# Kernel optimization log

Hardware: AMD Instinct MI355X
Metric: run time of the kernel (lower is better)

The kernel has to match this reference:

```python
import jax, jax.numpy as jnp
import numpy as np

B, N, C = 2, 2048, 768
H, HD = 12, 64
HID = 3072
LN_EPS = 1e-5
POL_EPS = 1e-6


def _layer_norm(x, g, b):
    m = jnp.mean(x, axis=-1, keepdims=True)
    v = jnp.mean(jnp.square(x - m), axis=-1, keepdims=True)
    return (x - m) * jax.lax.rsqrt(v + LN_EPS) * g + b


def _softmax_with_policy(attn, policy):
    # attn: [B,H,N,N], policy: [B,N,1]
    n = attn.shape[-1]
    ap = policy.reshape(policy.shape[0], 1, 1, n)  # [B,1,1,N]
    eye = jnp.eye(n, dtype=ap.dtype)[None, None]   # [1,1,N,N]
    ap = ap + (1.0 - ap) * eye                     # always attend to self
    attn = attn - jnp.max(attn, axis=-1, keepdims=True)
    attn = jnp.exp(attn.astype(jnp.float32)) * ap.astype(jnp.float32)
    attn = (attn + POL_EPS / n) / (jnp.sum(attn, axis=-1, keepdims=True) + POL_EPS)
    return attn


def setup_inputs() -> dict:
    key = jax.random.key(0)
    ks = jax.random.split(key, 12)
    s = lambda fan_in: 1.0 / np.sqrt(fan_in)
    x = jax.random.normal(ks[0], (B, N, C), dtype=jnp.float32)
    policy = (jax.random.uniform(ks[1], (B, N, 1)) > 0.5).astype(jnp.float32)
    return {
        "x": x,
        "policy": policy,
        "ln1_g": jnp.ones((C,), jnp.float32),
        "ln1_b": jnp.zeros((C,), jnp.float32),
        "qkv_w": jax.random.uniform(ks[2], (3 * H * HD, C), jnp.float32, -s(C), s(C)),
        "proj_w": jax.random.uniform(ks[3], (C, H * HD), jnp.float32, -s(H * HD), s(H * HD)),
        "proj_b": jnp.zeros((C,), jnp.float32),
        "ln2_g": jnp.ones((C,), jnp.float32),
        "ln2_b": jnp.zeros((C,), jnp.float32),
        "fc1_w": jax.random.uniform(ks[4], (HID, C), jnp.float32, -s(C), s(C)),
        "fc1_b": jnp.zeros((HID,), jnp.float32),
        "fc2_w": jax.random.uniform(ks[5], (C, HID), jnp.float32, -s(HID), s(HID)),
        "fc2_b": jnp.zeros((C,), jnp.float32),
    }


def reference(x, policy, ln1_g, ln1_b, qkv_w, proj_w, proj_b, ln2_g, ln2_b, fc1_w, fc1_b, fc2_w, fc2_b):
    b, n, c = x.shape
    scale = HD ** -0.5
    # --- attention branch (pre-LN) ---
    h = _layer_norm(x, ln1_g, ln1_b)
    qkv = (h @ qkv_w.T).reshape(b, n, 3, H, HD).transpose(2, 0, 3, 1, 4)  # [3,B,H,N,hd]
    q, k, v = qkv[0], qkv[1], qkv[2]
    attn = jnp.einsum("bhqd,bhkd->bhqk", q * scale, k)
    attn = _softmax_with_policy(attn, policy).astype(x.dtype)
    o = jnp.einsum("bhqk,bhkd->bhqd", attn, v).transpose(0, 2, 1, 3).reshape(b, n, H * HD)
    x = x + (o @ proj_w.T + proj_b)  # skip_lam = 1.0, dropout/drop_path = identity
    # --- MLP branch (pre-LN) ---
    h = _layer_norm(x, ln2_g, ln2_b)
    h = jax.nn.gelu(h @ fc1_w.T + fc1_b, approximate=False)  # torch nn.GELU = exact erf
    x = x + (h @ fc2_w.T + fc2_b)
    return x
```

## Files before the change

kernel.cpp:

```cpp
#include <hip/hip_runtime.h>

typedef unsigned short u16;
typedef unsigned int u32;
typedef float f32x4 __attribute__((ext_vector_type(4)));
typedef __bf16 bf16x8 __attribute__((ext_vector_type(8)));
typedef __bf16 bf16x4v __attribute__((ext_vector_type(4)));
typedef u16 u16x4v __attribute__((ext_vector_type(4)));
typedef u32 u32x2 __attribute__((ext_vector_type(2)));
typedef u32 u32x4 __attribute__((ext_vector_type(4)));

#define NHEAD 12
#define NN 2048
#define CC 768

#define GLOBAL_AS __attribute__((address_space(1)))
#define LDS_AS __attribute__((address_space(3)))

__device__ __forceinline__ u16 tobf(float f) {
  __bf16 h = (__bf16)f;
  return __builtin_bit_cast(u16, h);
}
__device__ __forceinline__ float bf2f(u16 h) {
  u32 u = ((u32)h) << 16;
  return __builtin_bit_cast(float, u);
}

#define N4_QKV 442368
#define N4_PROJ 147456
#define N4_FC 589824
__global__ __launch_bounds__(256) void cvt4_kernel(
    const float* __restrict__ a, const float* __restrict__ b,
    const float* __restrict__ c, const float* __restrict__ d,
    u16* __restrict__ oa, u16* __restrict__ ob, u16* __restrict__ oc,
    u16* __restrict__ od) {
  int i = blockIdx.x * 256 + threadIdx.x;
  const float* src;
  u16* dst;
  if (i < N4_QKV) {
    src = a; dst = oa;
  } else if (i < N4_QKV + N4_PROJ) {
    i -= N4_QKV; src = b; dst = ob;
  } else if (i < N4_QKV + N4_PROJ + N4_FC) {
    i -= N4_QKV + N4_PROJ; src = c; dst = oc;
  } else {
    i -= N4_QKV + N4_PROJ + N4_FC; src = d; dst = od;
    if (i >= N4_FC) return;
  }
  float4 v = ((const float4*)src)[i];
  u16x4v o = {tobf(v.x), tobf(v.y), tobf(v.z), tobf(v.w)};
  ((u16x4v*)dst)[i] = o;
}

__global__ __launch_bounds__(256) void ln_kernel(const float* __restrict__ x,
                                                 const float* __restrict__ gw,
                                                 const float* __restrict__ bw,
                                                 u16* __restrict__ out) {
  int row = blockIdx.x * 4 + (threadIdx.x >> 6);
  int lane = threadIdx.x & 63;
  const float* xr = x + (size_t)row * CC + lane * 12;
  float v[12];
  *(float4*)&v[0] = *(const float4*)(xr + 0);
  *(float4*)&v[4] = *(const float4*)(xr + 4);
  *(float4*)&v[8] = *(const float4*)(xr + 8);
  float s = 0.f, sq = 0.f;
#pragma unroll
  for (int j = 0; j < 12; ++j) { s += v[j]; sq += v[j] * v[j]; }
#pragma unroll
  for (int o = 1; o < 64; o <<= 1) { s += __shfl_xor(s, o); sq += __shfl_xor(sq, o); }
  float mean = s * (1.f / CC);
  float var = sq * (1.f / CC) - mean * mean;
  float rs = rsqrtf(var + 1e-5f);
  u16 ob[12];
#pragma unroll
  for (int j = 0; j < 12; ++j) {
    int c = lane * 12 + j;
    ob[j] = tobf((v[j] - mean) * rs * gw[c] + bw[c]);
  }
  u32* orow = (u32*)(out + (size_t)row * CC + lane * 12);
#pragma unroll
  for (int j = 0; j < 6; ++j) orow[j] = (u32)ob[2 * j] | ((u32)ob[2 * j + 1] << 16);
}

template <int BM, int OB, int HASB, int ACT, int RES>
__global__ __launch_bounds__(256) void gemm_kernel(
    const u16* __restrict__ A, const u16* __restrict__ Bw,
    const float* __restrict__ bias, const float* __restrict__ res,
    void* __restrict__ Cout, int M, int N, int K) {
  constexpr int MW = BM / 2;
  constexpr int MF = MW / 16;
  __shared__ __align__(16) u16 Alds[BM * 64];
  __shared__ __align__(16) u16 Blds[128 * 64];
  const int tid = threadIdx.x;
  const int lane = tid & 63, wave = tid >> 6;
  const int l15 = lane & 15, g = lane >> 4;
  const int bm = blockIdx.x * BM, bn = blockIdx.y * 128;
  const int wm = (wave >> 1) * MW, wn = (wave & 1) * 64;
  f32x4 acc[MF][4] = {};

  for (int kt = 0; kt < K; kt += 64) {
#pragma unroll
    for (int i = 0; i < BM / 32; ++i) {
      int ob_ = i * 4096 + wave * 1024;
      int lb = ob_ + lane * 16;
      int row = lb >> 7;
      int cb = (lb & 127) ^ ((row & 7) << 4);
      const u16* sa = A + (size_t)(bm + row) * K + kt + (cb >> 1);
      __builtin_amdgcn_global_load_lds((const GLOBAL_AS void*)sa,
                                       (LDS_AS void*)(Alds + (ob_ >> 1)), 16, 0, 0);
    }
#pragma unroll
    for (int i = 0; i < 4; ++i) {
      int ob_ = i * 4096 + wave * 1024;
      int lb = ob_ + lane * 16;
      int row = lb >> 7;
      int cb = (lb & 127) ^ ((row & 7) << 4);
      const u16* sb = Bw + (size_t)(bn + row) * K + kt + (cb >> 1);
      __builtin_amdgcn_global_load_lds((const GLOBAL_AS void*)sb,
                                       (LDS_AS void*)(Blds + (ob_ >> 1)), 16, 0, 0);
    }
    __syncthreads();
#pragma unroll
    for (int ks = 0; ks < 2; ++ks) {
      bf16x8 af[MF], bfr[4];
#pragma unroll
      for (int mi = 0; mi < MF; ++mi) {
        int row = wm + mi * 16 + l15;
        int cb = (ks * 64 + g * 16) ^ ((row & 7) << 4);
        af[mi] = *(const bf16x8*)&Alds[row * 64 + (cb >> 1)];
      }
#pragma unroll
      for (int ni = 0; ni < 4; ++ni) {
        int row = wn + ni * 16 + l15;
        int cb = (ks * 64 + g * 16) ^ ((row & 7) << 4);
        bfr[ni] = *(const bf16x8*)&Blds[row * 64 + (cb >> 1)];
      }
#pragma unroll
      for (int mi = 0; mi < MF; ++mi)
#pragma unroll
        for (int ni = 0; ni < 4; ++ni)
          acc[mi][ni] = __builtin_amdgcn_mfma_f32_16x16x32_bf16(af[mi], bfr[ni],
                                                                acc[mi][ni], 0, 0, 0);
    }
    __syncthreads();
  }
#pragma unroll
  for (int mi = 0; mi < MF; ++mi) {
#pragma unroll
    for (int ni = 0; ni < 4; ++ni) {
      int col = bn + wn + ni * 16 + l15;
      float bs = HASB ? bias[col] : 0.f;
#pragma unroll
      for (int r = 0; r < 4; ++r) {
        int rowm = bm + wm + mi * 16 + g * 4 + r;
        float v = acc[mi][ni][r] + bs;
        if (ACT) v = 0.5f * v * (1.f + erff(v * 0.70710678118654752f));
        if (RES) v += res[(size_t)rowm * N + col];
        if (OB)
          ((u16*)Cout)[(size_t)rowm * N + col] = tobf(v);
        else
          ((float*)Cout)[(size_t)rowm * N + col] = v;
      }
    }
  }
}

__global__ __launch_bounds__(256) void vsum_kernel(const u16* __restrict__ qkv,
                                                   float* __restrict__ vs) {
  int bh = blockIdx.x, q4 = blockIdx.y;
  int b = bh / NHEAD, h = bh % NHEAD;
  int d = threadIdx.x & 63, part = threadIdx.x >> 6;
  float s = 0.f;
  for (int n = q4 * 512 + part; n < q4 * 512 + 512; n += 4)
    s += bf2f(qkv[(size_t)(b * NN + n) * 2304 + 2 * CC + h * 64 + d]);
  __shared__ float red[256];
  red[threadIdx.x] = s;
  __syncthreads();
  if (threadIdx.x < 64) {
    float t = red[threadIdx.x] + red[threadIdx.x + 64] + red[threadIdx.x + 128] +
              red[threadIdx.x + 192];
    vs[q4 * (24 * 64) + bh * 64 + threadIdx.x] = t;
  }
}

#define SCL2E 0.18033688f
__global__ __launch_bounds__(256) void attn_kernel(const u16* __restrict__ qkv,
                                                   const float* __restrict__ policy,
                                                   const float* __restrict__ vsum,
                                                   u16* __restrict__ o) {
  __shared__ __align__(16) u16 Klds[2][64 * 64];
  __shared__ __align__(16) u16 Vlds[2][64 * 64];
  __shared__ __align__(16) u16 Plds[4][16 * 64];
  __shared__ float pol_lds[NN];
  const int bh = blockIdx.y, b = bh / NHEAD, h = bh % NHEAD;
  const int qtile = blockIdx.x * 64;
  const int tid = threadIdx.x, lane = tid & 63, w = tid >> 6;
  const int l15 = lane & 15, g = lane >> 4;
  const int qbase = qtile + w * 16;

  bf16x8 qf0, qf1;
  {
    const u16* qp = qkv + (size_t)(b * NN + qbase + l15) * 2304 + h * 64 + g * 8;
    bf16x8 r0 = *(const bf16x8*)qp;
    bf16x8 r1 = *(const bf16x8*)(qp + 32);
#pragma unroll
    for (int j = 0; j < 8; ++j) {
      qf0[j] = (__bf16)((float)r0[j] * SCL2E);
      qf1[j] = (__bf16)((float)r1[j] * SCL2E);
    }
  }

  const int I0 = w * 128 + lane, I1 = I0 + 64;
  const int kr0 = I0 >> 3, kc0 = (((I0 & 7) * 16) ^ ((kr0 & 7) << 4)) >> 1;
  const int kr1 = I1 >> 3, kc1 = (((I1 & 7) * 16) ^ ((kr1 & 7) << 4)) >> 1;
  const int vr0 = (I0 >> 5) * 4 + ((I0 & 7) >> 1), vc0 = ((I0 & 31) >> 3) * 16 + (I0 & 1) * 8;
  const int vr1 = (I1 >> 5) * 4 + ((I1 & 7) >> 1), vc1 = ((I1 & 31) >> 3) * 16 + (I1 & 1) * 8;
  const u16* pkA = qkv + (size_t)(b * NN + kr0) * 2304 + CC + h * 64 + kc0;
  const u16* pkB = qkv + (size_t)(b * NN + kr1) * 2304 + CC + h * 64 + kc1;
  const u16* pvA = qkv + (size_t)(b * NN + vr0) * 2304 + 2 * CC + h * 64 + vc0;
  const u16* pvB = qkv + (size_t)(b * NN + vr1) * 2304 + 2 * CC + h * 64 + vc1;
  const size_t adv = (size_t)64 * 2304;

  auto stage = [&](int buf) {
    __builtin_amdgcn_global_load_lds((const GLOBAL_AS void*)pkA,
                                     (LDS_AS void*)&Klds[buf][(w * 2 + 0) * 512], 16, 0, 0);
    __builtin_amdgcn_global_load_lds((const GLOBAL_AS void*)pkB,
                                     (LDS_AS void*)&Klds[buf][(w * 2 + 1) * 512], 16, 0, 0);
    __builtin_amdgcn_global_load_lds((const GLOBAL_AS void*)pvA,
                                     (LDS_AS void*)&Vlds[buf][(w * 2 + 0) * 512], 16, 0, 0);
    __builtin_amdgcn_global_load_lds((const GLOBAL_AS void*)pvB,
                                     (LDS_AS void*)&Vlds[buf][(w * 2 + 1) * 512], 16, 0, 0);
    pkA += adv; pkB += adv; pvA += adv; pvB += adv;
  };

  stage(0);
  {
    float4 p0 = *(const float4*)&policy[b * NN + tid * 8];
    float4 p1 = *(const float4*)&policy[b * NN + tid * 8 + 4];
    *(float4*)&pol_lds[tid * 8] = p0;
    *(float4*)&pol_lds[tid * 8 + 4] = p1;
  }
  __syncthreads();

  float m_cur = -3.0e38f, m_true = -3.0e38f, l_run = 0.f;
  f32x4 acc_o[4] = {};
  const u32 vbase0 = (u32)(uintptr_t)(LDS_AS u16*)&Vlds[0][0] + (u32)(g * 1024 + l15 * 2);
  const int qglob = qbase + l15;

  for (int t = 0; t < 32; ++t) {
    const int cur = t & 1;
    const int kv = t * 64;
    if (t < 31) stage(cur ^ 1);

    float sv[16];
#pragma unroll
    for (int kf = 0; kf < 4; ++kf) {
      int row = kf * 16 + l15;
      int sw = (row & 7) << 4;
      bf16x8 k0 = *(const bf16x8*)&Klds[cur][row * 64 + (((g * 16) ^ sw) >> 1)];
      bf16x8 k1 = *(const bf16x8*)&Klds[cur][row * 64 + (((64 + g * 16) ^ sw) >> 1)];
      f32x4 tacc = {};
      tacc = __builtin_amdgcn_mfma_f32_16x16x32_bf16(k0, qf0, tacc, 0, 0, 0);
      tacc = __builtin_amdgcn_mfma_f32_16x16x32_bf16(k1, qf1, tacc, 0, 0, 0);
#pragma unroll
      for (int r = 0; r < 4; ++r) sv[kf * 4 + r] = tacc[r];
    }
    float tmax = sv[0];
#pragma unroll
    for (int j = 1; j < 16; ++j) tmax = fmaxf(tmax, sv[j]);
    tmax = fmaxf(tmax, __shfl_xor(tmax, 16));
    tmax = fmaxf(tmax, __shfl_xor(tmax, 32));
    m_true = fmaxf(m_true, tmax);
    const bool defer = __all(tmax <= m_cur + 8.f);
    const float m_new = defer ? m_cur : fmaxf(m_cur, tmax);
    float psum = 0.f;
    bf16x4v pbk[4];
#pragma unroll
    for (int kf = 0; kf < 4; ++kf) {
      float4 pol4 = *(const float4*)&pol_lds[kv + kf * 16 + g * 4];
#pragma unroll
      for (int r = 0; r < 4; ++r) {
        int key = kv + kf * 16 + g * 4 + r;
        float ap = (key == qglob) ? 1.f : ((const float*)&pol4)[r];
        float e = exp2f(sv[kf * 4 + r] - m_new) * ap;
        psum += e;
        pbk[kf][r] = (__bf16)e;
      }
    }
    psum += __shfl_xor(psum, 16);
    psum += __shfl_xor(psum, 32);
    if (!defer) {
      float alpha = exp2f(m_cur - m_new);
      l_run = l_run * alpha + psum;
      m_cur = m_new;
      float ar0 = __shfl(alpha, g * 4 + 0);
      float ar1 = __shfl(alpha, g * 4 + 1);
      float ar2 = __shfl(alpha, g * 4 + 2);
      float ar3 = __shfl(alpha, g * 4 + 3);
#pragma unroll
      for (int df = 0; df < 4; ++df) {
        acc_o[df][0] *= ar0; acc_o[df][1] *= ar1;
        acc_o[df][2] *= ar2; acc_o[df][3] *= ar3;
      }
    } else {
      l_run += psum;
    }
#pragma unroll
    for (int kf = 0; kf < 4; ++kf) {
      int cb = (kf * 32 + g * 8) ^ ((l15 & 7) << 4);
      *(bf16x4v*)&Plds[w][l15 * 64 + (cb >> 1)] = pbk[kf];
    }
    u32x2 tr[2][4][2];
    const u32 vab = vbase0 + (u32)(cur * 8192);
#pragma unroll
    for (int ks = 0; ks < 2; ++ks)
#pragma unroll
      for (int df = 0; df < 4; ++df) {
        u32 va = vab + ks * 4096 + df * 128;
        asm volatile("ds_read_b64_tr_b16 %0, %1 offset:0" : "=v"(tr[ks][df][0]) : "v"(va));
        asm volatile("ds_read_b64_tr_b16 %0, %1 offset:512" : "=v"(tr[ks][df][1]) : "v"(va));
      }
    asm volatile("s_waitcnt lgkmcnt(0)" ::: "memory");
    __builtin_amdgcn_sched_barrier(0);
#pragma unroll
    for (int ks = 0; ks < 2; ++ks) {
      int cbp = (ks * 64 + g * 16) ^ ((l15 & 7) << 4);
      bf16x8 pf = *(const bf16x8*)&Plds[w][l15 * 64 + (cbp >> 1)];
#pragma unroll
      for (int df = 0; df < 4; ++df) {
        u32x4 tmp = {tr[ks][df][0].x, tr[ks][df][0].y, tr[ks][df][1].x, tr[ks][df][1].y};
        bf16x8 vf = __builtin_bit_cast(bf16x8, tmp);
        acc_o[df] = __builtin_amdgcn_mfma_f32_16x16x32_bf16(pf, vf, acc_o[df], 0, 0, 0);
      }
    }
    __syncthreads();
  }
  float s_adj = exp2f(m_cur - m_true);
  float lr[4], sr[4];
#pragma unroll
  for (int r = 0; r < 4; ++r) {
    lr[r] = __shfl(l_run, g * 4 + r);
    sr[r] = __shfl(s_adj, g * 4 + r);
  }
  const float epsn = 1e-6f / (float)NN;
#pragma unroll
  for (int df = 0; df < 4; ++df) {
    int d = df * 16 + l15;
    float vsv = vsum[bh * 64 + d] + vsum[1536 + bh * 64 + d] +
                vsum[2 * 1536 + bh * 64 + d] + vsum[3 * 1536 + bh * 64 + d];
#pragma unroll
    for (int r = 0; r < 4; ++r) {
      float ov = (acc_o[df][r] * sr[r] + epsn * vsv) / (lr[r] * sr[r] + 1e-6f);
      int qg = qbase + g * 4 + r;
      o[(size_t)(b * NN + qg) * CC + h * 64 + d] = tobf(ov);
    }
  }
}

extern "C" void kernel_launch(void* const* d_in, const int* in_sizes, int n_in,
                              void* d_out, int out_size, void* d_ws, size_t ws_size,
                              hipStream_t stream) {
  const float* x = (const float*)d_in[0];
  const float* policy = (const float*)d_in[1];
  const float* ln1g = (const float*)d_in[2];
  const float* ln1b = (const float*)d_in[3];
  const float* qkvw = (const float*)d_in[4];
  const float* projw = (const float*)d_in[5];
  const float* projb = (const float*)d_in[6];
  const float* ln2g = (const float*)d_in[7];
  const float* ln2b = (const float*)d_in[8];
  const float* fc1w = (const float*)d_in[9];
  const float* fc1b = (const float*)d_in[10];
  const float* fc2w = (const float*)d_in[11];
  const float* fc2b = (const float*)d_in[12];
  float* out = (float*)d_out;

  char* ws = (char*)d_ws;
  size_t off = 0;
  auto alloc = [&](size_t bytes) {
    void* p = ws + off;
    off = (off + bytes + 255) & ~(size_t)255;
    return p;
  };
  u16* wq = (u16*)alloc((size_t)2304 * 768 * 2);
  u16* wp = (u16*)alloc((size_t)768 * 768 * 2);
  u16* w1 = (u16*)alloc((size_t)3072 * 768 * 2);
  u16* w2 = (u16*)alloc((size_t)768 * 3072 * 2);
  u16* hbuf = (u16*)alloc((size_t)4096 * 768 * 2);
  u16* qkv = (u16*)alloc((size_t)4096 * 2304 * 2);
  u16* obuf = (u16*)alloc((size_t)4096 * 768 * 2);
  float* x1 = (float*)alloc((size_t)4096 * 768 * 4);
  float* vs = (float*)alloc((size_t)4 * 24 * 64 * 4);
  u16* f1 = qkv;

  cvt4_kernel<<<6912, 256, 0, stream>>>(qkvw, projw, fc1w, fc2w, wq, wp, w1, w2);

  ln_kernel<<<1024, 256, 0, stream>>>(x, ln1g, ln1b, hbuf);
  gemm_kernel<128, 1, 0, 0, 0><<<dim3(32, 18), 256, 0, stream>>>(
      hbuf, wq, nullptr, nullptr, qkv, 4096, 2304, 768);
  vsum_kernel<<<dim3(24, 4), 256, 0, stream>>>(qkv, vs);
  attn_kernel<<<dim3(32, 24), 256, 0, stream>>>(qkv, policy, vs, obuf);
  gemm_kernel<64, 0, 1, 0, 1><<<dim3(64, 6), 256, 0, stream>>>(
      obuf, wp, projb, x, x1, 4096, 768, 768);
  ln_kernel<<<1024, 256, 0, stream>>>(x1, ln2g, ln2b, hbuf);
  gemm_kernel<128, 1, 1, 1, 0><<<dim3(32, 24), 256, 0, stream>>>(
      hbuf, w1, fc1b, nullptr, f1, 4096, 3072, 768);
  gemm_kernel<64, 0, 1, 0, 1><<<dim3(64, 6), 256, 0, stream>>>(
      f1, w2, fc2b, x1, out, 4096, 768, 3072);
}
```

Measured before the change: 252.6 us.

## Rewrite attention with 32x32 MFMA, split-KV halves, and merge kernel

The attention kernel now uses 32x32x16 MFMA tiles, with each wave covering 32 queries. P is kept in registers through permlane32 swaps instead of being staged through LDS, and policy is stored in LDS as bf16. The key range is split into two halves across blocks, and each block writes an fp32 partial output plus l/m, which a new merge kernel combines with the epsilon term. The aim is fewer LDS round-trips and less per-instruction overhead, at the cost of extra global traffic for the partials and one more kernel launch.

```diff
diff --git a/kernel.cpp b/kernel.cpp
--- a/kernel.cpp
+++ b/kernel.cpp
@@ -3,8 +3,8 @@
 typedef unsigned short u16;
 typedef unsigned int u32;
 typedef float f32x4 __attribute__((ext_vector_type(4)));
+typedef float f32x16 __attribute__((ext_vector_type(16)));
 typedef __bf16 bf16x8 __attribute__((ext_vector_type(8)));
-typedef __bf16 bf16x4v __attribute__((ext_vector_type(4)));
 typedef u16 u16x4v __attribute__((ext_vector_type(4)));
 typedef u32 u32x2 __attribute__((ext_vector_type(2)));
 typedef u32 u32x4 __attribute__((ext_vector_type(4)));
@@ -23,6 +23,12 @@
 __device__ __forceinline__ float bf2f(u16 h) {
   u32 u = ((u32)h) << 16;
   return __builtin_bit_cast(float, u);
+}
+__device__ __forceinline__ void plswap(u32& a, u32& b) {
+  asm volatile("v_permlane32_swap_b32 %0, %1" : "+v"(a), "+v"(b));
+}
+__device__ __forceinline__ void plswapf(float& a, float& b) {
+  asm volatile("v_permlane32_swap_b32 %0, %1" : "+v"(a), "+v"(b));
 }
 
 #define N4_QKV 442368
@@ -183,177 +189,269 @@
 }
 
 #define SCL2E 0.18033688f
-__global__ __launch_bounds__(256) void attn_kernel(const u16* __restrict__ qkv,
-                                                   const float* __restrict__ policy,
-                                                   const float* __restrict__ vsum,
-                                                   u16* __restrict__ o) {
-  __shared__ __align__(16) u16 Klds[2][64 * 64];
-  __shared__ __align__(16) u16 Vlds[2][64 * 64];
-  __shared__ __align__(16) u16 Plds[4][16 * 64];
-  __shared__ float pol_lds[NN];
+#define TRRD(dst, addr, OFF) \
+  asm volatile("ds_read_b64_tr_b16 %0, %1 offset:" OFF : "=v"(dst) : "v"(addr))
+
+__global__ __launch_bounds__(256) void attn32_kernel(const u16* __restrict__ qkv,
+                                                     const float* __restrict__ policy,
+                                                     float* __restrict__ partO,
+                                                     float* __restrict__ partlm) {
+  __shared__ __align__(16) u16 Klds[2][4096];
+  __shared__ __align__(16) u16 Vlds[2][4096];
+  __shared__ u16 PolB[NN];
+  __shared__ float alf[4][32];
   const int bh = blockIdx.y, b = bh / NHEAD, h = bh % NHEAD;
-  const int qtile = blockIdx.x * 64;
+  const int qt = blockIdx.x >> 1, half = blockIdx.x & 1;
   const int tid = threadIdx.x, lane = tid & 63, w = tid >> 6;
-  const int l15 = lane & 15, g = lane >> 4;
-  const int qbase = qtile + w * 16;
-
-  bf16x8 qf0, qf1;
+  const int l31 = lane & 31, hp = lane >> 5, b4 = (lane >> 4) & 1;
+  const int q0 = qt * 128 + w * 32;
+  const int dv = q0 >> 6;
+  const int ktd = (q0 >> 5) & 1;
+  const int kv0 = half * 1024;
+  const size_t adv = (size_t)64 * 2304;
+
+  bf16x8 qf0, qf1, qf2, qf3;
   {
-    const u16* qp = qkv + (size_t)(b * NN + qbase + l15) * 2304 + h * 64 + g * 8;
-    bf16x8 r0 = *(const bf16x8*)qp;
-    bf16x8 r1 = *(const bf16x8*)(qp + 32);
-#pragma unroll
-    for (int j = 0; j < 8; ++j) {
-      qf0[j] = (__bf16)((float)r0[j] * SCL2E);
-      qf1[j] = (__bf16)((float)r1[j] * SCL2E);
-    }
-  }
-
-  const int I0 = w * 128 + lane, I1 = I0 + 64;
-  const int kr0 = I0 >> 3, kc0 = (((I0 & 7) * 16) ^ ((kr0 & 7) << 4)) >> 1;
-  const int kr1 = I1 >> 3, kc1 = (((I1 & 7) * 16) ^ ((kr1 & 7) << 4)) >> 1;
-  const int vr0 = (I0 >> 5) * 4 + ((I0 & 7) >> 1), vc0 = ((I0 & 31) >> 3) * 16 + (I0 & 1) * 8;
-  const int vr1 = (I1 >> 5) * 4 + ((I1 & 7) >> 1), vc1 = ((I1 & 31) >> 3) * 16 + (I1 & 1) * 8;
-  const u16* pkA = qkv + (size_t)(b * NN + kr0) * 2304 + CC + h * 64 + kc0;
-  const u16* pkB = qkv + (size_t)(b * NN + kr1) * 2304 + CC + h * 64 + kc1;
-  const u16* pvA = qkv + (size_t)(b * NN + vr0) * 2304 + 2 * CC + h * 64 + vc0;
-  const u16* pvB = qkv + (size_t)(b * NN + vr1) * 2304 + 2 * CC + h * 64 + vc1;
-  const size_t adv = (size_t)64 * 2304;
-
+    const u16* qp = qkv + (size_t)(b * NN + q0 + l31) * 2304 + h * 64 + 8 * hp;
+#pragma unroll
+    for (int ds = 0; ds < 4; ++ds) {
+      bf16x8 r = *(const bf16x8*)(qp + ds * 16);
+      bf16x8 o;
+#pragma unroll
+      for (int j = 0; j < 8; ++j) o[j] = (__bf16)((float)r[j] * SCL2E);
+      if (ds == 0) qf0 = o; else if (ds == 1) qf1 = o; else if (ds == 2) qf2 = o; else qf3 = o;
+    }
+  }
+
+  const u16* ksrc[2];
+  const u16* vsrcp[2];
+#pragma unroll
+  for (int c = 0; c < 2; ++c) {
+    int lb = c * 4096 + w * 1024 + lane * 16;
+    int row = lb >> 7;
+    int cb = (lb & 127) ^ ((row & 7) << 4);
+    ksrc[c] = qkv + (size_t)(b * NN + kv0 + row) * 2304 + CC + h * 64 + (cb >> 1);
+    int idx0 = (c * 256 + w * 64 + lane) * 8;
+    int s0 = idx0 & 15, jj = (idx0 >> 4) & 3, b4v = (idx0 >> 6) & 1,
+        pv = (idx0 >> 7) & 1, hv = (idx0 >> 8) & 1, dtv = (idx0 >> 9) & 1,
+        mkv = (idx0 >> 10) & 3;
+    int key = mkv * 16 + 8 * hv + 4 * pv + jj;
+    int d0 = dtv * 32 + 16 * b4v + s0;
+    vsrcp[c] = qkv + (size_t)(b * NN + kv0 + key) * 2304 + 2 * CC + h * 64 + d0;
+  }
   auto stage = [&](int buf) {
-    __builtin_amdgcn_global_load_lds((const GLOBAL_AS void*)pkA,
-                                     (LDS_AS void*)&Klds[buf][(w * 2 + 0) * 512], 16, 0, 0);
-    __builtin_amdgcn_global_load_lds((const GLOBAL_AS void*)pkB,
-                                     (LDS_AS void*)&Klds[buf][(w * 2 + 1) * 512], 16, 0, 0);
-    __builtin_amdgcn_global_load_lds((const GLOBAL_AS void*)pvA,
-                                     (LDS_AS void*)&Vlds[buf][(w * 2 + 0) * 512], 16, 0, 0);
-    __builtin_amdgcn_global_load_lds((const GLOBAL_AS void*)pvB,
-                                     (LDS_AS void*)&Vlds[buf][(w * 2 + 1) * 512], 16, 0, 0);
-    pkA += adv; pkB += adv; pvA += adv; pvB += adv;
+#pragma unroll
+    for (int c = 0; c < 2; ++c) {
+      __builtin_amdgcn_global_load_lds((const GLOBAL_AS void*)ksrc[c],
+                                       (LDS_AS void*)&Klds[buf][c * 2048 + w * 512], 16, 0, 0);
+      __builtin_amdgcn_global_load_lds((const GLOBAL_AS void*)vsrcp[c],
+                                       (LDS_AS void*)&Vlds[buf][c * 2048 + w * 512], 16, 0, 0);
+      ksrc[c] += adv; vsrcp[c] += adv;
+    }
   };
 
   stage(0);
   {
     float4 p0 = *(const float4*)&policy[b * NN + tid * 8];
     float4 p1 = *(const float4*)&policy[b * NN + tid * 8 + 4];
-    *(float4*)&pol_lds[tid * 8] = p0;
-    *(float4*)&pol_lds[tid * 8 + 4] = p1;
+    u16x4v a = {tobf(p0.x), tobf(p0.y), tobf(p0.z), tobf(p0.w)};
+    u16x4v c2 = {tobf(p1.x), tobf(p1.y), tobf(p1.z), tobf(p1.w)};
+    *(u16x4v*)&PolB[tid * 8] = a;
+    *(u16x4v*)&PolB[tid * 8 + 4] = c2;
   }
   __syncthreads();
 
   float m_cur = -3.0e38f, m_true = -3.0e38f, l_run = 0.f;
-  f32x4 acc_o[4] = {};
-  const u32 vbase0 = (u32)(uintptr_t)(LDS_AS u16*)&Vlds[0][0] + (u32)(g * 1024 + l15 * 2);
-  const int qglob = qbase + l15;
-
-  for (int t = 0; t < 32; ++t) {
+  f32x16 accd[2] = {};
+  const u32 vbase = (u32)(uintptr_t)(LDS_AS u16*)&Vlds[0][0] +
+                    (u32)(2 * (lane & 15) + 128 * b4 + 512 * hp);
+
+  for (int t = 0; t < 16; ++t) {
     const int cur = t & 1;
-    const int kv = t * 64;
-    if (t < 31) stage(cur ^ 1);
-
-    float sv[16];
-#pragma unroll
-    for (int kf = 0; kf < 4; ++kf) {
-      int row = kf * 16 + l15;
-      int sw = (row & 7) << 4;
-      bf16x8 k0 = *(const bf16x8*)&Klds[cur][row * 64 + (((g * 16) ^ sw) >> 1)];
-      bf16x8 k1 = *(const bf16x8*)&Klds[cur][row * 64 + (((64 + g * 16) ^ sw) >> 1)];
-      f32x4 tacc = {};
-      tacc = __builtin_amdgcn_mfma_f32_16x16x32_bf16(k0, qf0, tacc, 0, 0, 0);
-      tacc = __builtin_amdgcn_mfma_f32_16x16x32_bf16(k1, qf1, tacc, 0, 0, 0);
-#pragma unroll
-      for (int r = 0; r < 4; ++r) sv[kf * 4 + r] = tacc[r];
-    }
-    float tmax = sv[0];
-#pragma unroll
-    for (int j = 1; j < 16; ++j) tmax = fmaxf(tmax, sv[j]);
-    tmax = fmaxf(tmax, __shfl_xor(tmax, 16));
-    tmax = fmaxf(tmax, __shfl_xor(tmax, 32));
+    const int kvg = kv0 + t * 64;
+    if (t < 15) stage(cur ^ 1);
+
+    f32x16 sv0, sv1;
+    {
+      bf16x8 kf[4];
+#pragma unroll
+      for (int ds = 0; ds < 4; ++ds) {
+        int row = l31;
+        int cb = (32 * ds + 16 * hp) ^ ((row & 7) << 4);
+        kf[ds] = *(const bf16x8*)((const char*)&Klds[cur][0] + row * 128 + cb);
+      }
+      f32x16 a = {};
+      a = __builtin_amdgcn_mfma_f32_32x32x16_bf16(kf[0], qf0, a, 0, 0, 0);
+      a = __builtin_amdgcn_mfma_f32_32x32x16_bf16(kf[1], qf1, a, 0, 0, 0);
+      a = __builtin_amdgcn_mfma_f32_32x32x16_bf16(kf[2], qf2, a, 0, 0, 0);
+      a = __builtin_amdgcn_mfma_f32_32x32x16_bf16(kf[3], qf3, a, 0, 0, 0);
+      sv0 = a;
+    }
+    {
+      bf16x8 kf[4];
+#pragma unroll
+      for (int ds = 0; ds < 4; ++ds) {
+        int row = 32 + l31;
+        int cb = (32 * ds + 16 * hp) ^ ((row & 7) << 4);
+        kf[ds] = *(const bf16x8*)((const char*)&Klds[cur][0] + row * 128 + cb);
+      }
+      f32x16 a = {};
+      a = __builtin_amdgcn_mfma_f32_32x32x16_bf16(kf[0], qf0, a, 0, 0, 0);
+      a = __builtin_amdgcn_mfma_f32_32x32x16_bf16(kf[1], qf1, a, 0, 0, 0);
+      a = __builtin_amdgcn_mfma_f32_32x32x16_bf16(kf[2], qf2, a, 0, 0, 0);
+      a = __builtin_amdgcn_mfma_f32_32x32x16_bf16(kf[3], qf3, a, 0, 0, 0);
+      sv1 = a;
+    }
+
+    u32x2 tr[4][2][2];
+    {
+      u32 vab = vbase + (u32)(cur * 8192);
+      TRRD(tr[0][0][0], vab, "0");    TRRD(tr[0][0][1], vab, "256");
+      TRRD(tr[0][1][0], vab, "1024"); TRRD(tr[0][1][1], vab, "1280");
+      TRRD(tr[1][0][0], vab, "2048"); TRRD(tr[1][0][1], vab, "2304");
+      TRRD(tr[1][1][0], vab, "3072"); TRRD(tr[1][1][1], vab, "3328");
+      TRRD(tr[2][0][0], vab, "4096"); TRRD(tr[2][0][1], vab, "4352");
+      TRRD(tr[3][0][0], vab, "6144"); TRRD(tr[3][0][1], vab, "6400");
+      TRRD(tr[2][1][0], vab, "5120"); TRRD(tr[2][1][1], vab, "5376");
+      TRRD(tr[3][1][0], vab, "7168"); TRRD(tr[3][1][1], vab, "7424");
+    }
+
+    float tmax = sv0[0];
+#pragma unroll
+    for (int r = 1; r < 16; ++r) tmax = fmaxf(tmax, sv0[r]);
+#pragma unroll
+    for (int r = 0; r < 16; ++r) tmax = fmaxf(tmax, sv1[r]);
+    {
+      float t1 = tmax, t2 = tmax;
+      plswapf(t1, t2);
+      tmax = fmaxf(t1, t2);
+    }
     m_true = fmaxf(m_true, tmax);
     const bool defer = __all(tmax <= m_cur + 8.f);
     const float m_new = defer ? m_cur : fmaxf(m_cur, tmax);
+
+    const bool isdiag = ((half * 16 + t) == dv);
+    u16 pb[32];
     float psum = 0.f;
-    bf16x4v pbk[4];
-#pragma unroll
-    for (int kf = 0; kf < 4; ++kf) {
-      float4 pol4 = *(const float4*)&pol_lds[kv + kf * 16 + g * 4];
-#pragma unroll
-      for (int r = 0; r < 4; ++r) {
-        int key = kv + kf * 16 + g * 4 + r;
-        float ap = (key == qglob) ? 1.f : ((const float*)&pol4)[r];
-        float e = exp2f(sv[kf * 4 + r] - m_new) * ap;
-        psum += e;
-        pbk[kf][r] = (__bf16)e;
-      }
-    }
-    psum += __shfl_xor(psum, 16);
-    psum += __shfl_xor(psum, 32);
+#pragma unroll
+    for (int kt = 0; kt < 2; ++kt) {
+#pragma unroll
+      for (int i = 0; i < 4; ++i) {
+        u16x4v pq = *(const u16x4v*)&PolB[kvg + kt * 32 + 8 * i + 4 * hp];
+#pragma unroll
+        for (int rq = 0; rq < 4; ++rq) {
+          int r = 4 * i + rq;
+          float ap = bf2f(pq[rq]);
+          if (isdiag && kt == ktd) ap = ((8 * i + 4 * hp + rq) == l31) ? 1.f : ap;
+          float sval = kt ? sv1[r] : sv0[r];
+          float e = exp2f(sval - m_new) * ap;
+          u16 eb = tobf(e);
+          psum += bf2f(eb);
+          pb[kt * 16 + r] = eb;
+        }
+      }
+    }
+    {
+      float s1 = psum, s2 = psum;
+      plswapf(s1, s2);
+      psum = s1 + s2;
+    }
     if (!defer) {
       float alpha = exp2f(m_cur - m_new);
       l_run = l_run * alpha + psum;
       m_cur = m_new;
-      float ar0 = __shfl(alpha, g * 4 + 0);
-      float ar1 = __shfl(alpha, g * 4 + 1);
-      float ar2 = __shfl(alpha, g * 4 + 2);
-      float ar3 = __shfl(alpha, g * 4 + 3);
-#pragma unroll
-      for (int df = 0; df < 4; ++df) {
-        acc_o[df][0] *= ar0; acc_o[df][1] *= ar1;
-        acc_o[df][2] *= ar2; acc_o[df][3] *= ar3;
+      if (lane < 32) alf[w][lane] = alpha;
+      float4 aq0 = *(const float4*)&alf[w][4 * hp];
+      float4 aq1 = *(const float4*)&alf[w][8 + 4 * hp];
+      float4 aq2 = *(const float4*)&alf[w][16 + 4 * hp];
+      float4 aq3 = *(const float4*)&alf[w][24 + 4 * hp];
+#pragma unroll
+      for (int dt = 0; dt < 2; ++dt) {
+#pragma unroll
+        for (int rq = 0; rq < 4; ++rq) {
+          accd[dt][0 + rq] *= ((const float*)&aq0)[rq];
+          accd[dt][4 + rq] *= ((const float*)&aq1)[rq];
+          accd[dt][8 + rq] *= ((const float*)&aq2)[rq];
+          accd[dt][12 + rq] *= ((const float*)&aq3)[rq];
+        }
       }
     } else {
       l_run += psum;
     }
-#pragma unroll
-    for (int kf = 0; kf < 4; ++kf) {
-      int cb = (kf * 32 + g * 8) ^ ((l15 & 7) << 4);
-      *(bf16x4v*)&Plds[w][l15 * 64 + (cb >> 1)] = pbk[kf];
-    }
-    u32x2 tr[2][4][2];
-    const u32 vab = vbase0 + (u32)(cur * 8192);
-#pragma unroll
-    for (int ks = 0; ks < 2; ++ks)
-#pragma unroll
-      for (int df = 0; df < 4; ++df) {
-        u32 va = vab + ks * 4096 + df * 128;
-        asm volatile("ds_read_b64_tr_b16 %0, %1 offset:0" : "=v"(tr[ks][df][0]) : "v"(va));
-        asm volatile("ds_read_b64_tr_b16 %0, %1 offset:512" : "=v"(tr[ks][df][1]) : "v"(va));
-      }
+
+    u32 PK[4][4];
+#pragma unroll
+    for (int mk = 0; mk < 4; ++mk) {
+      int bs = 16 * (mk >> 1) + 8 * (mk & 1);
+      PK[mk][0] = (u32)pb[bs + 0] | ((u32)pb[bs + 1] << 16);
+      PK[mk][1] = (u32)pb[bs + 2] | ((u32)pb[bs + 3] << 16);
+      PK[mk][2] = (u32)pb[bs + 4] | ((u32)pb[bs + 5] << 16);
+      PK[mk][3] = (u32)pb[bs + 6] | ((u32)pb[bs + 7] << 16);
+      plswap(PK[mk][2], PK[mk][0]);
+      plswap(PK[mk][3], PK[mk][1]);
+    }
+
     asm volatile("s_waitcnt lgkmcnt(0)" ::: "memory");
     __builtin_amdgcn_sched_barrier(0);
-#pragma unroll
-    for (int ks = 0; ks < 2; ++ks) {
-      int cbp = (ks * 64 + g * 16) ^ ((l15 & 7) << 4);
-      bf16x8 pf = *(const bf16x8*)&Plds[w][l15 * 64 + (cbp >> 1)];
-#pragma unroll
-      for (int df = 0; df < 4; ++df) {
-        u32x4 tmp = {tr[ks][df][0].x, tr[ks][df][0].y, tr[ks][df][1].x, tr[ks][df][1].y};
-        bf16x8 vf = __builtin_bit_cast(bf16x8, tmp);
-        acc_o[df] = __builtin_amdgcn_mfma_f32_16x16x32_bf16(pf, vf, acc_o[df], 0, 0, 0);
+
+#pragma unroll
+    for (int mk = 0; mk < 4; ++mk) {
+      u32x4 pk4 = {PK[mk][0], PK[mk][1], PK[mk][2], PK[mk][3]};
+      bf16x8 pf = __builtin_bit_cast(bf16x8, pk4);
+#pragma unroll
+      for (int dt = 0; dt < 2; ++dt) {
+        u32x4 vv = {tr[mk][dt][0].x, tr[mk][dt][0].y, tr[mk][dt][1].x, tr[mk][dt][1].y};
+        bf16x8 vf = __builtin_bit_cast(bf16x8, vv);
+        accd[dt] = __builtin_amdgcn_mfma_f32_32x32x16_bf16(pf, vf, accd[dt], 0, 0, 0);
       }
     }
     __syncthreads();
   }
-  float s_adj = exp2f(m_cur - m_true);
-  float lr[4], sr[4];
-#pragma unroll
-  for (int r = 0; r < 4; ++r) {
-    lr[r] = __shfl(l_run, g * 4 + r);
-    sr[r] = __shfl(s_adj, g * 4 + r);
-  }
-  const float epsn = 1e-6f / (float)NN;
-#pragma unroll
-  for (int df = 0; df < 4; ++df) {
-    int d = df * 16 + l15;
-    float vsv = vsum[bh * 64 + d] + vsum[1536 + bh * 64 + d] +
-                vsum[2 * 1536 + bh * 64 + d] + vsum[3 * 1536 + bh * 64 + d];
-#pragma unroll
-    for (int r = 0; r < 4; ++r) {
-      float ov = (acc_o[df][r] * sr[r] + epsn * vsv) / (lr[r] * sr[r] + 1e-6f);
-      int qg = qbase + g * 4 + r;
-      o[(size_t)(b * NN + qg) * CC + h * 64 + d] = tobf(ov);
-    }
-  }
+
+  float sr = exp2f(m_cur - m_true);
+  if (lane < 32) {
+    alf[w][lane] = sr;
+    float2 lm = {l_run * sr, m_true};
+    *(float2*)&partlm[2 * ((size_t)(half * 24 + bh) * 2048 + q0 + lane)] = lm;
+  }
+  float4 sq0 = *(const float4*)&alf[w][4 * hp];
+  float4 sq1 = *(const float4*)&alf[w][8 + 4 * hp];
+  float4 sq2 = *(const float4*)&alf[w][16 + 4 * hp];
+  float4 sq3 = *(const float4*)&alf[w][24 + 4 * hp];
+  float* pb2 = partO + ((size_t)(half * 24 + bh) * 2048) * 64;
+#pragma unroll
+  for (int dt = 0; dt < 2; ++dt) {
+#pragma unroll
+    for (int i = 0; i < 4; ++i) {
+      float4 sqv = (i == 0) ? sq0 : (i == 1) ? sq1 : (i == 2) ? sq2 : sq3;
+#pragma unroll
+      for (int rq = 0; rq < 4; ++rq) {
+        int row = q0 + 8 * i + 4 * hp + rq;
+        pb2[(size_t)row * 64 + dt * 32 + l31] = accd[dt][4 * i + rq] * ((const float*)&sqv)[rq];
+      }
+    }
+  }
+}
+
+__global__ __launch_bounds__(256) void merge_kernel(const float* __restrict__ partO,
+                                                    const float* __restrict__ partlm,
+                                                    const float* __restrict__ vs,
+                                                    u16* __restrict__ o) {
+  int rr = blockIdx.x * 4 + (threadIdx.x >> 6);
+  int lane = threadIdx.x & 63;
+  int bh = rr >> 11, q = rr & 2047;
+  int b = bh / NHEAD, h = bh % NHEAD;
+  const float* O1 = partO + ((size_t)bh * 2048 + q) * 64;
+  const float* O2 = partO + ((size_t)(24 + bh) * 2048 + q) * 64;
+  float2 lm1 = ((const float2*)partlm)[(size_t)bh * 2048 + q];
+  float2 lm2 = ((const float2*)partlm)[(size_t)(24 + bh) * 2048 + q];
+  float ms = fmaxf(lm1.y, lm2.y);
+  float w1 = exp2f(lm1.y - ms), w2 = exp2f(lm2.y - ms);
+  float den = lm1.x * w1 + lm2.x * w2 + 1e-6f;
+  float vsv = vs[bh * 64 + lane] + vs[1536 + bh * 64 + lane] +
+              vs[3072 + bh * 64 + lane] + vs[4608 + bh * 64 + lane];
+  float num = O1[lane] * w1 + O2[lane] * w2 + (1e-6f / 2048.f) * vsv;
+  o[((size_t)(b * NN + q)) * CC + h * 64 + lane] = tobf(num / den);
 }
 
 extern "C" void kernel_launch(void* const* d_in, const int* in_sizes, int n_in,
@@ -388,8 +486,11 @@
   u16* hbuf = (u16*)alloc((size_t)4096 * 768 * 2);
   u16* qkv = (u16*)alloc((size_t)4096 * 2304 * 2);
   u16* obuf = (u16*)alloc((size_t)4096 * 768 * 2);
-  float* x1 = (float*)alloc((size_t)4096 * 768 * 4);
   float* vs = (float*)alloc((size_t)4 * 24 * 64 * 4);
+  size_t unionOff = off;
+  float* partO = (float*)alloc((size_t)2 * 24 * 2048 * 64 * 4);
+  float* partlm = (float*)alloc((size_t)2 * 24 * 2048 * 2 * 4);
+  float* x1 = (float*)(ws + unionOff);
   u16* f1 = qkv;
 
   cvt4_kernel<<<6912, 256, 0, stream>>>(qkvw, projw, fc1w, fc2w, wq, wp, w1, w2);
@@ -398,7 +499,8 @@
   gemm_kernel<128, 1, 0, 0, 0><<<dim3(32, 18), 256, 0, stream>>>(
       hbuf, wq, nullptr, nullptr, qkv, 4096, 2304, 768);
   vsum_kernel<<<dim3(24, 4), 256, 0, stream>>>(qkv, vs);
-  attn_kernel<<<dim3(32, 24), 256, 0, stream>>>(qkv, policy, vs, obuf);
+  attn32_kernel<<<dim3(32, 24), 256, 0, stream>>>(qkv, policy, partO, partlm);
+  merge_kernel<<<12288, 256, 0, stream>>>(partO, partlm, vs, obuf);
   gemm_kernel<64, 0, 1, 0, 1><<<dim3(64, 6), 256, 0, stream>>>(
       obuf, wp, projb, x, x1, 4096, 768, 768);
   ln_kernel<<<1024, 256, 0, stream>>>(x1, ln2g, ln2b, hbuf);
```

New measurement: 254.4 us. About the same (+0.7%).
